# Optimization experiments

Measured on AMD Instinct MI355X. Metric: run time of the kernel, lower is better.

The kernel has to match this reference:

```python
import jax, jax.numpy as jnp
import numpy as np

BLK = 46  # hardcoded block size in the original module
EPS = 1e-5


def setup_inputs() -> dict:
    key = jax.random.key(0)
    ks = jax.random.split(key, 13)
    N, C, Ci = 128, 512, 256
    return {
        "ori_feature": jax.random.normal(ks[0], (N, C, BLK), jnp.float32),
        "bn_gamma": jax.random.uniform(ks[1], (C,), jnp.float32),
        "bn_beta": jax.random.normal(ks[2], (C,), jnp.float32),
        "bn_mean": jax.random.normal(ks[3], (C,), jnp.float32),
        "bn_var": jax.random.uniform(ks[4], (C,), jnp.float32),
        "theta_w": jax.random.normal(ks[5], (Ci, C), jnp.float32) * 0.02,
        "theta_b": jax.random.normal(ks[6], (Ci,), jnp.float32) * 0.02,
        "phi_w": jax.random.normal(ks[7], (Ci, C), jnp.float32) * 0.02,
        "phi_b": jax.random.normal(ks[8], (Ci,), jnp.float32) * 0.02,
        "g_w": jax.random.normal(ks[9], (Ci, C), jnp.float32) * 0.02,
        "g_b": jax.random.normal(ks[10], (Ci,), jnp.float32) * 0.02,
        "W_w": jax.random.normal(ks[11], (C, Ci), jnp.float32) * 0.02,
        "W_b": jax.random.normal(ks[12], (C,), jnp.float32) * 0.02,
    }


def reference(ori_feature, bn_gamma, bn_beta, bn_mean, bn_var,
              theta_w, theta_b, phi_w, phi_b, g_w, g_b, W_w, W_b):
    N, C, num = ori_feature.shape  # (N, C, 46)
    # BatchNorm1d (inference-style, per-channel) + ReLU
    inv = bn_gamma / jnp.sqrt(bn_var + EPS)
    feat = jax.nn.relu(ori_feature * inv[None, :, None]
                       + (bn_beta - bn_mean * inv)[None, :, None])
    feat = feat.transpose(0, 2, 1).reshape(N * num, C)  # (T, C)
    x_theta = feat @ theta_w.T + theta_b  # (T, Ci)
    x_phi = feat @ phi_w.T + phi_b        # (T, Ci)
    attn = x_theta @ x_phi.T              # (T, T)
    # block-diagonal masking: entries within the same 46-token block set to -1000
    blk = jnp.arange(N * num) // num
    attn = jnp.where(blk[:, None] == blk[None, :], jnp.float32(-1000.0), attn)
    f_div_C = jax.nn.softmax(attn, axis=-1)
    g_x = feat @ g_w.T + g_b              # (T, Ci)
    y = f_div_C @ g_x                     # (T, Ci)
    W_y = (y @ W_w.T + W_b).reshape(N, num, C)
    att_fea = ori_feature.transpose(0, 2, 1) + W_y  # (N, 46, C)
    return att_fea, f_div_C
```

## Files before the change

### kernel.cpp

```cpp
#include <hip/hip_runtime.h>
#include <math.h>

#define N_BATCH 128
#define C_DIM   512
#define BLKSZ   46
#define T_DIM   (N_BATCH * BLKSZ)
#define CI      256
#define EPS_BN  1e-5f
#define NCB     (T_DIM / 128)

typedef __attribute__((ext_vector_type(8))) short bf16x8;
typedef __attribute__((ext_vector_type(4))) float f32x4;

__device__ __forceinline__ short f2bf(float f) {
    union { float f; unsigned u; } v; v.f = f;
    unsigned r = v.u + 0x7fffu + ((v.u >> 16) & 1u);
    return (short)(r >> 16);
}

__device__ __forceinline__ float h2f(unsigned short h) {
    _Float16 x; __builtin_memcpy(&x, &h, 2); return (float)x;
}
__device__ __forceinline__ unsigned short f2h(float f) {
    _Float16 x = (_Float16)f; unsigned short u; __builtin_memcpy(&u, &x, 2); return u;
}

__device__ __forceinline__ void gload16(const void* g, void* l) {
    __builtin_amdgcn_global_load_lds((__attribute__((address_space(1))) void*)g,
                                     (__attribute__((address_space(3))) void*)l,
                                     16, 0, 0);
}

__global__ __launch_bounds__(256) void bn_relu_kernel(
    const float* __restrict__ ori, const float* __restrict__ gamma,
    const float* __restrict__ beta, const float* __restrict__ mean,
    const float* __restrict__ var, short* __restrict__ feat)
{
    __shared__ short tile[256 * BLKSZ];
    const int n = blockIdx.y;
    const int c0 = blockIdx.x * 256;
    const int tid = threadIdx.x;
    for (int i = tid; i < 256 * BLKSZ; i += 256) {
        int cl = i / BLKSZ, b = i - cl * BLKSZ;
        int c = c0 + cl;
        float inv = gamma[c] * rsqrtf(var[c] + EPS_BN);
        float v = ori[((size_t)n * C_DIM + c) * BLKSZ + b] * inv + (beta[c] - mean[c] * inv);
        tile[cl * BLKSZ + b] = f2bf(fmaxf(v, 0.0f));
    }
    __syncthreads();
    for (int i = tid; i < BLKSZ * 256; i += 256) {
        int b = i >> 8, cl = i & 255;
        feat[(size_t)(n * BLKSZ + b) * C_DIM + c0 + cl] = tile[cl * BLKSZ + b];
    }
}

__global__ __launch_bounds__(256) void cvt_kernel(
    const float* __restrict__ thw, const float* __restrict__ phw,
    const float* __restrict__ gw, const float* __restrict__ Ww,
    const float* __restrict__ thb, const float* __restrict__ phb,
    short* __restrict__ wcat, short* __restrict__ wg,
    short* __restrict__ wW, float* __restrict__ bcat)
{
    const int i = blockIdx.x * 256 + threadIdx.x;
    const float* src[4] = {thw, phw, gw, Ww};
    short* dst[4] = {wcat, wcat + 256 * 512, wg, wW};
    #pragma unroll
    for (int m = 0; m < 4; ++m) {
        float4 v = *(const float4*)(src[m] + (size_t)i * 4);
        short4 t = make_short4(f2bf(v.x), f2bf(v.y), f2bf(v.z), f2bf(v.w));
        *(short4*)(dst[m] + (size_t)i * 4) = t;
    }
    if (blockIdx.x == 0) {
        bcat[threadIdx.x] = thb[threadIdx.x];
        bcat[threadIdx.x + 256] = phb[threadIdx.x];
    }
}

template <int EPI, int ACVT, int BM, int BN>
__global__ __launch_bounds__(256, 2) void gemm_nt(
    const void* __restrict__ Avoid, const short* __restrict__ B,
    const float* __restrict__ bias, void* __restrict__ Cvoid,
    int M, int Nn, int K, int lda, int ldb, int nsplit,
    const float* __restrict__ ori,
    float* __restrict__ stats, const float* __restrict__ rowstat,
    float* __restrict__ fout)
{
    constexpr int NWC = BN / 64;
    constexpr int NWR = 4 / NWC;
    constexpr int MI  = BM / (NWR * 16);
    static_assert((EPI != 5 && EPI != 6) || NWC == 2, "stats epilogue assumes NWC==2");
    __shared__ short As[BM * 32];
    __shared__ short Bs[BN * 32];
    const int tid = threadIdx.x;
    const int w = tid >> 6, lane = tid & 63;
    const int m0 = blockIdx.y * BM, n0 = blockIdx.x * BN;
    const int wr = w / NWC, wc = w % NWC;
    const int wrow = wr * (MI * 16);

    const int kper = K / 32 / nsplit;
    const int kt0 = blockIdx.z * kper, kt1 = kt0 + kper;

    f32x4 acc[MI][4] = {};

    const int sr = tid >> 2;
    const int sc = (tid & 3) * 8;
    const short* Ab = (const short*)Avoid;
    const float* Af = (const float*)Avoid;
    const unsigned short* Ah = (const unsigned short*)Avoid;

    float rm = 0.f, rz = 0.f;
    int a_r = 0, a_c = 0;
    if constexpr (ACVT != 0) {
        constexpr int EPT = BM * 32 / 256;
        constexpr int TPR = 32 / EPT;
        a_r = tid / TPR;
        a_c = (tid % TPR) * EPT;
        float2 st = ((const float2*)rowstat)[m0 + a_r];
        rm = st.x; rz = st.y;
    }

    for (int kt = kt0; kt < kt1; ++kt) {
        const int k0 = kt * 32;
        if constexpr (ACVT == 0) {
            #pragma unroll
            for (int p = 0; p < BM / 64; ++p)
                gload16(Ab + (size_t)(m0 + p * 64 + sr) * lda + k0 + sc,
                        &As[(p * 64 + sr) * 32 + sc]);
        } else {
            constexpr int EPT = BM * 32 / 256;
            const int k0c = k0 + a_c;
            float* fd = fout + (size_t)(m0 + a_r) * lda + k0c;
            short tmp[EPT] __attribute__((aligned(16)));
            #pragma unroll
            for (int q = 0; q < EPT / 4; ++q) {
                float4 e;
                if constexpr (ACVT == 1) {
                    float4 v = *(const float4*)(Af + (size_t)(m0 + a_r) * lda + k0c + q * 4);
                    e.x = expf(v.x - rm) * rz;
                    e.y = expf(v.y - rm) * rz;
                    e.z = expf(v.z - rm) * rz;
                    e.w = expf(v.w - rm) * rz;
                } else {
                    ushort4 hv = *(const ushort4*)(Ah + (size_t)(m0 + a_r) * lda + k0c + q * 4);
                    e.x = expf(h2f(hv.x) - rm) * rz;
                    e.y = expf(h2f(hv.y) - rm) * rz;
                    e.z = expf(h2f(hv.z) - rm) * rz;
                    e.w = expf(h2f(hv.w) - rm) * rz;
                }
                *(float4*)(fd + q * 4) = e;
                tmp[q * 4 + 0] = f2bf(e.x); tmp[q * 4 + 1] = f2bf(e.y);
                tmp[q * 4 + 2] = f2bf(e.z); tmp[q * 4 + 3] = f2bf(e.w);
            }
            #pragma unroll
            for (int q = 0; q < EPT / 4; ++q)
                *(short4*)&As[a_r * 32 + a_c + q * 4] = *(short4*)&tmp[q * 4];
        }
        #pragma unroll
        for (int p = 0; p < BN / 64; ++p)
            gload16(B + (size_t)(n0 + p * 64 + sr) * ldb + k0 + sc,
                    &Bs[(p * 64 + sr) * 32 + sc]);
        __syncthreads();

        bf16x8 af[MI], bfr[4];
        #pragma unroll
        for (int i = 0; i < MI; ++i)
            af[i] = *(bf16x8*)&As[(wrow + i * 16 + (lane & 15)) * 32 + (lane >> 4) * 8];
        #pragma unroll
        for (int j = 0; j < 4; ++j)
            bfr[j] = *(bf16x8*)&Bs[(wc * 64 + j * 16 + (lane & 15)) * 32 + (lane >> 4) * 8];
        #pragma unroll
        for (int i = 0; i < MI; ++i)
            #pragma unroll
            for (int j = 0; j < 4; ++j)
                acc[i][j] = __builtin_amdgcn_mfma_f32_16x16x32_bf16(af[i], bfr[j], acc[i][j], 0, 0, 0);
        __syncthreads();
    }

    const int col = lane & 15, rowq = lane >> 4;

    if constexpr (EPI == 5 || EPI == 6) {
        __shared__ float sm[NWC][BM];
        __shared__ float ss[NWC][BM];
        int cbj[4];
        #pragma unroll
        for (int j = 0; j < 4; ++j)
            cbj[j] = (n0 + wc * 64 + j * 16 + col) / BLKSZ;
        #pragma unroll
        for (int i = 0; i < MI; ++i) {
            #pragma unroll
            for (int r = 0; r < 4; ++r) {
                const int trow = wrow + i * 16 + rowq * 4 + r;
                const int grow = m0 + trow;
                const int rb = grow / BLKSZ;
                float vj[4];
                float vmax = -1e30f;
                #pragma unroll
                for (int j = 0; j < 4; ++j) {
                    float v = acc[i][j][r];
                    if (cbj[j] == rb) v = -30000.0f;
                    const size_t idx = (size_t)grow * Nn + (n0 + wc * 64 + j * 16 + col);
                    if constexpr (EPI == 6) {
                        unsigned short hh = f2h(v);
                        ((unsigned short*)Cvoid)[idx] = hh;
                        v = h2f(hh);
                    } else {
                        ((float*)Cvoid)[idx] = v;
                    }
                    vj[j] = v;
                    vmax = fmaxf(vmax, v);
                }
                #pragma unroll
                for (int off = 1; off < 16; off <<= 1)
                    vmax = fmaxf(vmax, __shfl_xor(vmax, off));
                float s = 0.f;
                #pragma unroll
                for (int j = 0; j < 4; ++j) s += expf(vj[j] - vmax);
                #pragma unroll
                for (int off = 1; off < 16; off <<= 1)
                    s += __shfl_xor(s, off);
                if (col == 0) { sm[wc][trow] = vmax; ss[wc][trow] = s; }
            }
        }
        __syncthreads();
        if (tid < BM) {
            const float ma = sm[0][tid], mb = sm[1][tid];
            const float mx = fmaxf(ma, mb);
            const float S = ss[0][tid] * expf(ma - mx) + ss[1][tid] * expf(mb - mx);
            ((float2*)stats)[(size_t)blockIdx.x * M + (m0 + tid)] = make_float2(mx, S);
        }
    } else {
        #pragma unroll
        for (int i = 0; i < MI; ++i) {
            #pragma unroll
            for (int j = 0; j < 4; ++j) {
                #pragma unroll
                for (int r = 0; r < 4; ++r) {
                    const int grow = m0 + wrow + i * 16 + rowq * 4 + r;
                    const int gcol = n0 + wc * 64 + j * 16 + col;
                    const float v = acc[i][j][r];
                    if (EPI == 1) {
                        ((short*)Cvoid)[(size_t)grow * Nn + gcol] = f2bf(v + bias[gcol]);
                    } else if (EPI == 2) {
                        ((short*)Cvoid)[(size_t)grow * Nn + gcol] = f2bf(v + bias[grow]);
                    } else if (EPI == 3) {
                        ((float*)Cvoid)[(size_t)blockIdx.z * M * Nn + (size_t)grow * Nn + gcol] = v;
                    } else {
                        const int nb = grow / BLKSZ, bb = grow - nb * BLKSZ;
                        ((float*)Cvoid)[(size_t)grow * Nn + gcol] =
                            v + bias[gcol] + ori[((size_t)nb * C_DIM + gcol) * BLKSZ + bb];
                    }
                }
            }
        }
    }
}

__global__ __launch_bounds__(256) void combine_stats_kernel(
    const float* __restrict__ stats, float* __restrict__ rowstat)
{
    const int row = blockIdx.x * 256 + threadIdx.x;
    float m = -1e30f, Z = 0.f;
    for (int cb = 0; cb < NCB; ++cb) {
        float2 p = ((const float2*)stats)[(size_t)cb * T_DIM + row];
        float nm = fmaxf(m, p.x);
        Z = Z * expf(m - nm) + p.y * expf(p.x - nm);
        m = nm;
    }
    ((float2*)rowstat)[row] = make_float2(m, 1.0f / Z);
}

__global__ __launch_bounds__(256) void reduce_y_kernel(
    const float* __restrict__ part, short* __restrict__ y, int ns)
{
    const size_t i = (size_t)blockIdx.x * 256 + threadIdx.x;
    float4 s = *(const float4*)(part + i * 4);
    for (int z = 1; z < ns; ++z) {
        float4 v = *(const float4*)(part + (size_t)z * T_DIM * CI + i * 4);
        s.x += v.x; s.y += v.y; s.z += v.z; s.w += v.w;
    }
    short4 t = make_short4(f2bf(s.x), f2bf(s.y), f2bf(s.z), f2bf(s.w));
    *(short4*)(y + i * 4) = t;
}

extern "C" void kernel_launch(void* const* d_in, const int* in_sizes, int n_in,
                              void* d_out, int out_size, void* d_ws, size_t ws_size,
                              hipStream_t stream)
{
    const float* ori     = (const float*)d_in[0];
    const float* gamma   = (const float*)d_in[1];
    const float* beta    = (const float*)d_in[2];
    const float* mean    = (const float*)d_in[3];
    const float* var     = (const float*)d_in[4];
    const float* theta_w = (const float*)d_in[5];
    const float* theta_b = (const float*)d_in[6];
    const float* phi_w   = (const float*)d_in[7];
    const float* phi_b   = (const float*)d_in[8];
    const float* g_w     = (const float*)d_in[9];
    const float* g_b     = (const float*)d_in[10];
    const float* W_w     = (const float*)d_in[11];
    const float* W_b     = (const float*)d_in[12];

    float* out = (float*)d_out;
    float* P   = out + (size_t)T_DIM * C_DIM;

    char* wsb = (char*)d_ws;
    short* feat = (short*)wsb;  wsb += (size_t)T_DIM * C_DIM * 2;
    short* xcat = (short*)wsb;  wsb += (size_t)T_DIM * 512 * 2;
    short* gxT  = (short*)wsb;  wsb += (size_t)CI * T_DIM * 2;
    short* wcat = (short*)wsb;  wsb += (size_t)512 * C_DIM * 2;
    short* wg   = (short*)wsb;  wsb += (size_t)CI * C_DIM * 2;
    short* wW   = (short*)wsb;  wsb += (size_t)C_DIM * CI * 2;
    float* bcat = (float*)wsb;  wsb += 512 * 4;
    short* ybf  = (short*)wsb;  wsb += (size_t)T_DIM * CI * 2;
    float* rowstat = (float*)wsb; wsb += (size_t)T_DIM * 8;

    const size_t base   = (size_t)(wsb - (char*)d_ws);
    const size_t p16sz  = (size_t)T_DIM * T_DIM * 2;
    const size_t ypsz4  = 4u * (size_t)T_DIM * CI * 4u;
    const bool bigws = ws_size >= base + p16sz + ypsz4;

    bn_relu_kernel<<<dim3(2, 128), 256, 0, stream>>>(ori, gamma, beta, mean, var, feat);
    cvt_kernel<<<128, 256, 0, stream>>>(theta_w, phi_w, g_w, W_w, theta_b, phi_b,
                                        wcat, wg, wW, bcat);

    gemm_nt<1, 0, 128, 128><<<dim3(4, T_DIM / 128), 256, 0, stream>>>(
        feat, wcat, bcat, xcat, T_DIM, 512, C_DIM, C_DIM, C_DIM, 1, nullptr,
        nullptr, nullptr, nullptr);

    gemm_nt<2, 0, 128, 128><<<dim3(T_DIM / 128, CI / 128), 256, 0, stream>>>(
        wg, feat, g_b, gxT, CI, T_DIM, C_DIM, C_DIM, C_DIM, 1, nullptr,
        nullptr, nullptr, nullptr);

    if (bigws) {
        unsigned short* p16 = (unsigned short*)wsb;
        float* ypart = (float*)(wsb + p16sz);
        float* stats = ypart;

        gemm_nt<6, 0, 128, 128><<<dim3(T_DIM / 128, T_DIM / 128), 256, 0, stream>>>(
            xcat, xcat + CI, nullptr, p16, T_DIM, T_DIM, CI, 512, 512, 1, nullptr,
            stats, nullptr, nullptr);
        combine_stats_kernel<<<T_DIM / 256, 256, 0, stream>>>(stats, rowstat);
        gemm_nt<3, 2, 32, 256><<<dim3(1, T_DIM / 32, 4), 256, 0, stream>>>(
            p16, gxT, nullptr, ypart, T_DIM, CI, T_DIM, T_DIM, T_DIM, 4, nullptr,
            nullptr, rowstat, P);
        reduce_y_kernel<<<(T_DIM * CI / 4) / 256, 256, 0, stream>>>(ypart, ybf, 4);
    } else {
        float* ypart = (float*)wsb;
        float* stats = ypart;
        const int ns = (ws_size >= base + ypsz4) ? 4 : 2;

        gemm_nt<5, 0, 128, 128><<<dim3(T_DIM / 128, T_DIM / 128), 256, 0, stream>>>(
            xcat, xcat + CI, nullptr, P, T_DIM, T_DIM, CI, 512, 512, 1, nullptr,
            stats, nullptr, nullptr);
        combine_stats_kernel<<<T_DIM / 256, 256, 0, stream>>>(stats, rowstat);
        gemm_nt<3, 1, 32, 256><<<dim3(1, T_DIM / 32, ns), 256, 0, stream>>>(
            P, gxT, nullptr, ypart, T_DIM, CI, T_DIM, T_DIM, T_DIM, ns, nullptr,
            nullptr, rowstat, P);
        reduce_y_kernel<<<(T_DIM * CI / 4) / 256, 256, 0, stream>>>(ypart, ybf, ns);
    }

    gemm_nt<4, 0, 128, 128><<<dim3(C_DIM / 128, T_DIM / 128), 256, 0, stream>>>(
        ybf, wW, W_b, out, T_DIM, C_DIM, CI, CI, CI, 1, ori,
        nullptr, nullptr, nullptr);
}
```

Before: 350.5 us.

## Pipeline softmax-P GEMM, fuse projection GEMMs, add XCD remap and occupancy

```diff
diff --git a/kernel.cpp b/kernel.cpp
--- a/kernel.cpp
+++ b/kernel.cpp
@@ -30,6 +30,9 @@
                                      (__attribute__((address_space(3))) void*)l,
                                      16, 0, 0);
 }
+
+template <int A> struct avec_sel { using t = float4; };
+template <> struct avec_sel<2> { using t = ushort4; };
 
 __global__ __launch_bounds__(256) void bn_relu_kernel(
     const float* __restrict__ ori, const float* __restrict__ gamma,
@@ -58,12 +61,12 @@
     const float* __restrict__ thw, const float* __restrict__ phw,
     const float* __restrict__ gw, const float* __restrict__ Ww,
     const float* __restrict__ thb, const float* __restrict__ phb,
-    short* __restrict__ wcat, short* __restrict__ wg,
-    short* __restrict__ wW, float* __restrict__ bcat)
+    const float* __restrict__ gb,
+    short* __restrict__ wall, short* __restrict__ wW, float* __restrict__ bcat)
 {
     const int i = blockIdx.x * 256 + threadIdx.x;
     const float* src[4] = {thw, phw, gw, Ww};
-    short* dst[4] = {wcat, wcat + 256 * 512, wg, wW};
+    short* dst[4] = {wall, wall + 256 * 512, wall + 512 * 512, wW};
     #pragma unroll
     for (int m = 0; m < 4; ++m) {
         float4 v = *(const float4*)(src[m] + (size_t)i * 4);
@@ -73,11 +76,12 @@
     if (blockIdx.x == 0) {
         bcat[threadIdx.x] = thb[threadIdx.x];
         bcat[threadIdx.x + 256] = phb[threadIdx.x];
-    }
-}
-
-template <int EPI, int ACVT, int BM, int BN>
-__global__ __launch_bounds__(256, 2) void gemm_nt(
+        bcat[threadIdx.x + 512] = gb[threadIdx.x];
+    }
+}
+
+template <int EPI, int ACVT, int BM, int BN, int OCC = 2>
+__global__ __launch_bounds__(256, OCC) void gemm_nt(
     const void* __restrict__ Avoid, const short* __restrict__ B,
     const float* __restrict__ bias, void* __restrict__ Cvoid,
     int M, int Nn, int K, int lda, int ldb, int nsplit,
@@ -88,12 +92,24 @@
     constexpr int NWC = BN / 64;
     constexpr int NWR = 4 / NWC;
     constexpr int MI  = BM / (NWR * 16);
-    static_assert((EPI != 5 && EPI != 6) || NWC == 2, "stats epilogue assumes NWC==2");
-    __shared__ short As[BM * 32];
-    __shared__ short Bs[BN * 32];
+    constexpr int NBUF = (ACVT != 0) ? 2 : 1;
+    static_assert((EPI != 5 && EPI != 6 && EPI != 7) || NWC == 2, "stats/split epilogue assumes NWC==2");
+    static_assert(ACVT == 0 || BN == 256, "pipelined vmcnt count assumes BN==256");
+    __shared__ short As[NBUF * BM * 32];
+    __shared__ short Bs[NBUF * BN * 32];
     const int tid = threadIdx.x;
     const int w = tid >> 6, lane = tid & 63;
-    const int m0 = blockIdx.y * BM, n0 = blockIdx.x * BN;
+
+    int bx = blockIdx.x, by = blockIdx.y;
+    if constexpr (EPI == 5 || EPI == 6) {
+        const int nwg = gridDim.x * gridDim.y;
+        const int orig = by * gridDim.x + bx;
+        const int q = nwg >> 3, r = nwg & 7;
+        const int xcd = orig & 7, idx = orig >> 3;
+        const int wg = (xcd < r ? xcd * (q + 1) : r * (q + 1) + (xcd - r) * q) + idx;
+        bx = wg % gridDim.x; by = wg / gridDim.x;
+    }
+    const int m0 = by * BM, n0 = bx * BN;
     const int wr = w / NWC, wc = w % NWC;
     const int wrow = wr * (MI * 16);
 
@@ -105,75 +121,94 @@
     const int sr = tid >> 2;
     const int sc = (tid & 3) * 8;
     const short* Ab = (const short*)Avoid;
-    const float* Af = (const float*)Avoid;
-    const unsigned short* Ah = (const unsigned short*)Avoid;
-
-    float rm = 0.f, rz = 0.f;
-    int a_r = 0, a_c = 0;
-    if constexpr (ACVT != 0) {
-        constexpr int EPT = BM * 32 / 256;
-        constexpr int TPR = 32 / EPT;
-        a_r = tid / TPR;
-        a_c = (tid % TPR) * EPT;
-        float2 st = ((const float2*)rowstat)[m0 + a_r];
-        rm = st.x; rz = st.y;
-    }
-
-    for (int kt = kt0; kt < kt1; ++kt) {
-        const int k0 = kt * 32;
-        if constexpr (ACVT == 0) {
+
+    if constexpr (ACVT == 0) {
+        for (int kt = kt0; kt < kt1; ++kt) {
+            const int k0 = kt * 32;
             #pragma unroll
             for (int p = 0; p < BM / 64; ++p)
                 gload16(Ab + (size_t)(m0 + p * 64 + sr) * lda + k0 + sc,
                         &As[(p * 64 + sr) * 32 + sc]);
-        } else {
-            constexpr int EPT = BM * 32 / 256;
-            const int k0c = k0 + a_c;
-            float* fd = fout + (size_t)(m0 + a_r) * lda + k0c;
-            short tmp[EPT] __attribute__((aligned(16)));
-            #pragma unroll
-            for (int q = 0; q < EPT / 4; ++q) {
-                float4 e;
-                if constexpr (ACVT == 1) {
-                    float4 v = *(const float4*)(Af + (size_t)(m0 + a_r) * lda + k0c + q * 4);
-                    e.x = expf(v.x - rm) * rz;
-                    e.y = expf(v.y - rm) * rz;
-                    e.z = expf(v.z - rm) * rz;
-                    e.w = expf(v.w - rm) * rz;
-                } else {
-                    ushort4 hv = *(const ushort4*)(Ah + (size_t)(m0 + a_r) * lda + k0c + q * 4);
-                    e.x = expf(h2f(hv.x) - rm) * rz;
-                    e.y = expf(h2f(hv.y) - rm) * rz;
-                    e.z = expf(h2f(hv.z) - rm) * rz;
-                    e.w = expf(h2f(hv.w) - rm) * rz;
-                }
-                *(float4*)(fd + q * 4) = e;
-                tmp[q * 4 + 0] = f2bf(e.x); tmp[q * 4 + 1] = f2bf(e.y);
-                tmp[q * 4 + 2] = f2bf(e.z); tmp[q * 4 + 3] = f2bf(e.w);
-            }
-            #pragma unroll
-            for (int q = 0; q < EPT / 4; ++q)
-                *(short4*)&As[a_r * 32 + a_c + q * 4] = *(short4*)&tmp[q * 4];
-        }
+            #pragma unroll
+            for (int p = 0; p < BN / 64; ++p)
+                gload16(B + (size_t)(n0 + p * 64 + sr) * ldb + k0 + sc,
+                        &Bs[(p * 64 + sr) * 32 + sc]);
+            __syncthreads();
+
+            bf16x8 af[MI], bfr[4];
+            #pragma unroll
+            for (int i = 0; i < MI; ++i)
+                af[i] = *(bf16x8*)&As[(wrow + i * 16 + (lane & 15)) * 32 + (lane >> 4) * 8];
+            #pragma unroll
+            for (int j = 0; j < 4; ++j)
+                bfr[j] = *(bf16x8*)&Bs[(wc * 64 + j * 16 + (lane & 15)) * 32 + (lane >> 4) * 8];
+            #pragma unroll
+            for (int i = 0; i < MI; ++i)
+                #pragma unroll
+                for (int j = 0; j < 4; ++j)
+                    acc[i][j] = __builtin_amdgcn_mfma_f32_16x16x32_bf16(af[i], bfr[j], acc[i][j], 0, 0, 0);
+            __syncthreads();
+        }
+    } else {
+        constexpr int EPT = BM * 32 / 256;
+        static_assert(EPT == 4, "pipelined ACVT path assumes EPT==4");
+        constexpr int TPR = 32 / EPT;
+        const int a_r = tid / TPR;
+        const int a_c = (tid % TPR) * EPT;
+        float2 st = ((const float2*)rowstat)[m0 + a_r];
+        const float rm = st.x, rz = st.y;
+        using AV = typename avec_sel<ACVT>::t;
+        const AV* Arow = (const AV*)((const char*)Avoid
+                         + ((size_t)(m0 + a_r) * lda) * (ACVT == 2 ? 2 : 4));
+        float* frow = fout + (size_t)(m0 + a_r) * lda;
+
+        AV hv = Arow[(kt0 * 32 + a_c) / 4];
         #pragma unroll
         for (int p = 0; p < BN / 64; ++p)
-            gload16(B + (size_t)(n0 + p * 64 + sr) * ldb + k0 + sc,
+            gload16(B + (size_t)(n0 + p * 64 + sr) * ldb + kt0 * 32 + sc,
                     &Bs[(p * 64 + sr) * 32 + sc]);
-        __syncthreads();
-
-        bf16x8 af[MI], bfr[4];
-        #pragma unroll
-        for (int i = 0; i < MI; ++i)
-            af[i] = *(bf16x8*)&As[(wrow + i * 16 + (lane & 15)) * 32 + (lane >> 4) * 8];
-        #pragma unroll
-        for (int j = 0; j < 4; ++j)
-            bfr[j] = *(bf16x8*)&Bs[(wc * 64 + j * 16 + (lane & 15)) * 32 + (lane >> 4) * 8];
-        #pragma unroll
-        for (int i = 0; i < MI; ++i)
+
+        for (int kt = kt0; kt < kt1; ++kt) {
+            const int cur = (kt - kt0) & 1;
+            const int kc = kt * 32 + a_c;
+            float4 vf;
+            if constexpr (ACVT == 2) {
+                vf.x = h2f(hv.x); vf.y = h2f(hv.y); vf.z = h2f(hv.z); vf.w = h2f(hv.w);
+            } else {
+                vf.x = hv.x; vf.y = hv.y; vf.z = hv.z; vf.w = hv.w;
+            }
+            float4 e;
+            e.x = expf(vf.x - rm) * rz; e.y = expf(vf.y - rm) * rz;
+            e.z = expf(vf.z - rm) * rz; e.w = expf(vf.w - rm) * rz;
+            *(float4*)(frow + kc) = e;
+            short4 t = make_short4(f2bf(e.x), f2bf(e.y), f2bf(e.z), f2bf(e.w));
+            *(short4*)&As[cur * BM * 32 + a_r * 32 + a_c] = t;
+
+            if (kt + 1 < kt1) {
+                hv = Arow[((kt + 1) * 32 + a_c) / 4];
+                #pragma unroll
+                for (int p = 0; p < BN / 64; ++p)
+                    gload16(B + (size_t)(n0 + p * 64 + sr) * ldb + (kt + 1) * 32 + sc,
+                            &Bs[(cur ^ 1) * BN * 32 + (p * 64 + sr) * 32 + sc]);
+                asm volatile("s_waitcnt vmcnt(6) lgkmcnt(0)\n\ts_barrier" ::: "memory");
+            } else {
+                asm volatile("s_waitcnt vmcnt(1) lgkmcnt(0)\n\ts_barrier" ::: "memory");
+            }
+
+            bf16x8 af[MI], bfr[4];
+            #pragma unroll
+            for (int i = 0; i < MI; ++i)
+                af[i] = *(bf16x8*)&As[cur * BM * 32 + (wrow + i * 16 + (lane & 15)) * 32 + (lane >> 4) * 8];
             #pragma unroll
             for (int j = 0; j < 4; ++j)
-                acc[i][j] = __builtin_amdgcn_mfma_f32_16x16x32_bf16(af[i], bfr[j], acc[i][j], 0, 0, 0);
-        __syncthreads();
+                bfr[j] = *(bf16x8*)&Bs[cur * BN * 32 + (wc * 64 + j * 16 + (lane & 15)) * 32 + (lane >> 4) * 8];
+            #pragma unroll
+            for (int i = 0; i < MI; ++i)
+                #pragma unroll
+                for (int j = 0; j < 4; ++j)
+                    acc[i][j] = __builtin_amdgcn_mfma_f32_16x16x32_bf16(af[i], bfr[j], acc[i][j], 0, 0, 0);
+            asm volatile("s_barrier" ::: "memory");
+        }
     }
 
     const int col = lane & 15, rowq = lane >> 4;
@@ -226,7 +261,35 @@
             const float ma = sm[0][tid], mb = sm[1][tid];
             const float mx = fmaxf(ma, mb);
             const float S = ss[0][tid] * expf(ma - mx) + ss[1][tid] * expf(mb - mx);
-            ((float2*)stats)[(size_t)blockIdx.x * M + (m0 + tid)] = make_float2(mx, S);
+            ((float2*)stats)[(size_t)bx * M + (m0 + tid)] = make_float2(mx, S);
+        }
+    } else if constexpr (EPI == 7) {
+        if (n0 < 512) {
+            #pragma unroll
+            for (int i = 0; i < MI; ++i)
+                #pragma unroll
+                for (int j = 0; j < 4; ++j)
+                    #pragma unroll
+                    for (int r = 0; r < 4; ++r) {
+                        const int grow = m0 + wrow + i * 16 + rowq * 4 + r;
+                        const int gcol = n0 + wc * 64 + j * 16 + col;
+                        ((short*)Cvoid)[(size_t)grow * 512 + gcol] =
+                            f2bf(acc[i][j][r] + bias[gcol]);
+                    }
+        } else {
+            short* gxTp = (short*)stats;
+            #pragma unroll
+            for (int i = 0; i < MI; ++i)
+                #pragma unroll
+                for (int j = 0; j < 4; ++j) {
+                    const int grow0 = m0 + wrow + i * 16 + rowq * 4;
+                    const int gcol = n0 + wc * 64 + j * 16 + col;
+                    const float bv = bias[gcol];
+                    short4 t = make_short4(
+                        f2bf(acc[i][j][0] + bv), f2bf(acc[i][j][1] + bv),
+                        f2bf(acc[i][j][2] + bv), f2bf(acc[i][j][3] + bv));
+                    *(short4*)&gxTp[(size_t)(gcol - 512) * T_DIM + grow0] = t;
+                }
         }
     } else {
         #pragma unroll
@@ -307,10 +370,9 @@
     short* feat = (short*)wsb;  wsb += (size_t)T_DIM * C_DIM * 2;
     short* xcat = (short*)wsb;  wsb += (size_t)T_DIM * 512 * 2;
     short* gxT  = (short*)wsb;  wsb += (size_t)CI * T_DIM * 2;
-    short* wcat = (short*)wsb;  wsb += (size_t)512 * C_DIM * 2;
-    short* wg   = (short*)wsb;  wsb += (size_t)CI * C_DIM * 2;
+    short* wall = (short*)wsb;  wsb += (size_t)768 * C_DIM * 2;
     short* wW   = (short*)wsb;  wsb += (size_t)C_DIM * CI * 2;
-    float* bcat = (float*)wsb;  wsb += 512 * 4;
+    float* bcat = (float*)wsb;  wsb += 768 * 4;
     short* ybf  = (short*)wsb;  wsb += (size_t)T_DIM * CI * 2;
     float* rowstat = (float*)wsb; wsb += (size_t)T_DIM * 8;
 
@@ -320,16 +382,12 @@
     const bool bigws = ws_size >= base + p16sz + ypsz4;
 
     bn_relu_kernel<<<dim3(2, 128), 256, 0, stream>>>(ori, gamma, beta, mean, var, feat);
-    cvt_kernel<<<128, 256, 0, stream>>>(theta_w, phi_w, g_w, W_w, theta_b, phi_b,
-                                        wcat, wg, wW, bcat);
-
-    gemm_nt<1, 0, 128, 128><<<dim3(4, T_DIM / 128), 256, 0, stream>>>(
-        feat, wcat, bcat, xcat, T_DIM, 512, C_DIM, C_DIM, C_DIM, 1, nullptr,
-        nullptr, nullptr, nullptr);
-
-    gemm_nt<2, 0, 128, 128><<<dim3(T_DIM / 128, CI / 128), 256, 0, stream>>>(
-        wg, feat, g_b, gxT, CI, T_DIM, C_DIM, C_DIM, C_DIM, 1, nullptr,
-        nullptr, nullptr, nullptr);
+    cvt_kernel<<<128, 256, 0, stream>>>(theta_w, phi_w, g_w, W_w, theta_b, phi_b, g_b,
+                                        wall, wW, bcat);
+
+    gemm_nt<7, 0, 128, 128><<<dim3(6, T_DIM / 128), 256, 0, stream>>>(
+        feat, wall, bcat, xcat, T_DIM, 768, C_DIM, C_DIM, C_DIM, 1, nullptr,
+        (float*)gxT, nullptr, nullptr);
 
     if (bigws) {
         unsigned short* p16 = (unsigned short*)wsb;
@@ -340,7 +398,7 @@
             xcat, xcat + CI, nullptr, p16, T_DIM, T_DIM, CI, 512, 512, 1, nullptr,
             stats, nullptr, nullptr);
         combine_stats_kernel<<<T_DIM / 256, 256, 0, stream>>>(stats, rowstat);
-        gemm_nt<3, 2, 32, 256><<<dim3(1, T_DIM / 32, 4), 256, 0, stream>>>(
+        gemm_nt<3, 2, 32, 256, 4><<<dim3(1, T_DIM / 32, 4), 256, 0, stream>>>(
             p16, gxT, nullptr, ypart, T_DIM, CI, T_DIM, T_DIM, T_DIM, 4, nullptr,
             nullptr, rowstat, P);
         reduce_y_kernel<<<(T_DIM * CI / 4) / 256, 256, 0, stream>>>(ypart, ybf, 4);
@@ -353,7 +411,7 @@
             xcat, xcat + CI, nullptr, P, T_DIM, T_DIM, CI, 512, 512, 1, nullptr,
             stats, nullptr, nullptr);
         combine_stats_kernel<<<T_DIM / 256, 256, 0, stream>>>(stats, rowstat);
-        gemm_nt<3, 1, 32, 256><<<dim3(1, T_DIM / 32, ns), 256, 0, stream>>>(
+        gemm_nt<3, 1, 32, 256, 4><<<dim3(1, T_DIM / 32, ns), 256, 0, stream>>>(
             P, gxT, nullptr, ypart, T_DIM, CI, T_DIM, T_DIM, T_DIM, ns, nullptr,
             nullptr, rowstat, P);
         reduce_y_kernel<<<(T_DIM * CI / 4) / 256, 256, 0, stream>>>(ypart, ybf, ns);
```

Measured after the change: 340.6 us. 2.8% less time.
